# Kernel optimization log

Hardware: AMD Instinct MI355X
Metric: run time of the kernel (lower is better)

## Reference

```python
import jax, jax.numpy as jnp
import numpy as np

N_NODES = 100000
N_EDGES = 1600000
D_IN = 64
D_OUT = 64


def setup_inputs() -> dict:
    key = jax.random.key(0)
    k1, k2, k3, k4, k5, k6 = jax.random.split(key, 6)
    feat = jax.random.normal(k1, (N_NODES, D_IN), dtype=jnp.float32)
    src = jax.random.randint(k2, (N_EDGES,), 0, N_NODES, dtype=jnp.int64)
    dst = jax.random.randint(k3, (N_EDGES,), 0, N_NODES, dtype=jnp.int64)
    edge_weight = jax.random.uniform(k4, (N_EDGES,), dtype=jnp.float32)
    # Xavier-uniform with relu gain, as in reset_parameters
    gain = float(np.sqrt(2.0))
    bound = gain * float(np.sqrt(6.0 / (D_IN + D_OUT)))
    W_neigh = jax.random.uniform(k5, (D_OUT, D_IN), dtype=jnp.float32, minval=-bound, maxval=bound)
    W_self = jax.random.uniform(k6, (D_OUT, D_IN), dtype=jnp.float32, minval=-bound, maxval=bound)
    bias = jnp.zeros((D_OUT,), dtype=jnp.float32)
    return {"feat": feat, "src": src, "dst": dst, "edge_weight": edge_weight,
            "W_neigh": W_neigh, "W_self": W_self, "bias": bias}


def reference(feat, src, dst, edge_weight, W_neigh, W_self, bias):
    n = feat.shape[0]
    # feat_drop with p=0.0 is identity; in_feats == out_feats so lin_before_mp is False
    # message: u_mul_e -> gather src features, scale by edge weight  [E, D_IN]
    m = feat[src] * edge_weight[:, None]
    # mean reduce over incoming edges (zero for isolated dst nodes, matching DGL)
    s = jax.ops.segment_sum(m, dst, num_segments=n)
    deg = jax.ops.segment_sum(jnp.ones_like(edge_weight), dst, num_segments=n)
    neigh = s / jnp.maximum(deg, 1.0)[:, None]
    h_neigh = neigh @ W_neigh.T
    h_self = feat @ W_self.T
    return h_self + h_neigh + bias
```

## Files before the change

### kernel.cpp

```cpp
#include <hip/hip_runtime.h>

constexpr int N_NODES = 100000;
constexpr int N_EDGES = 1600000;
constexpr int D = 64;

constexpr int BSH    = 6;
constexpr int BN     = 1 << BSH;
constexpr int NBUCK  = (N_NODES + BN - 1) / BN;
constexpr int NPART  = 200;
constexpr int EPB    = N_EDGES / NPART;
constexpr int CAP    = 2048;
constexpr int RMAX   = 512;
constexpr int NCVT   = (N_NODES * D / 4) / 256;

constexpr size_t OFF_NCUR    = 0;
constexpr size_t OFF_BCUR    = 400000;
constexpr size_t OFF_W16     = 409600;
constexpr size_t OFF_ENTRIES = 425984;
constexpr size_t OFF_FEAT16  = 26034176;
constexpr size_t WS_NEEDED   = OFF_FEAT16 + (size_t)N_NODES * D * 2;

typedef short  bf16x8 __attribute__((ext_vector_type(8)));
typedef float  f32x4  __attribute__((ext_vector_type(4)));

union FragU { unsigned u[4]; bf16x8 v; };

__device__ __forceinline__ unsigned short f2bf(float f) {
    unsigned u = __float_as_uint(f);
    u += 0x7fffu + ((u >> 16) & 1u);
    return (unsigned short)(u >> 16);
}

__global__ __launch_bounds__(256) void k_zero(int* __restrict__ ncur,
                                              int* __restrict__ bcur) {
    const int stride = gridDim.x * 256;
    for (int i = blockIdx.x * 256 + threadIdx.x; i < N_NODES; i += stride)
        ncur[i] = 0;
    for (int i = blockIdx.x * 256 + threadIdx.x; i < NBUCK; i += stride)
        bcur[i] = 0;
}

__global__ __launch_bounds__(256) void k_pre(const float4* __restrict__ feat4,
                                             unsigned short* __restrict__ feat16,
                                             const float* __restrict__ Wn,
                                             const float* __restrict__ Ws,
                                             unsigned short* __restrict__ W16) {
    const int b   = blockIdx.x;
    const int tid = threadIdx.x;
    if (b < NCVT) {
        const int i = b * 256 + tid;
        float4 v = feat4[i];
        ushort4 o;
        o.x = f2bf(v.x); o.y = f2bf(v.y); o.z = f2bf(v.z); o.w = f2bf(v.w);
        *(ushort4*)&feat16[(size_t)i * 4] = o;
    } else {
        for (int e = tid; e < D * 128; e += 256) {
            const int j = e >> 7, k = e & 127;
            const float w = (k < D) ? Ws[j * D + k] : Wn[j * D + (k - D)];
            W16[e] = f2bf(w);
        }
    }
}

__global__ __launch_bounds__(256) void k_part(const int* __restrict__ src,
                                              const int* __restrict__ dst,
                                              const float* __restrict__ ew,
                                              int* __restrict__ ncur,
                                              int* __restrict__ bcur,
                                              uint2* __restrict__ entries) {
    __shared__ int l[NBUCK];
    const int tid  = threadIdx.x;
    const int base = blockIdx.x * EPB;
    for (int i = tid; i < NBUCK; i += 256) l[i] = 0;
    __syncthreads();
    for (int k = tid; k < EPB; k += 256)
        atomicAdd(&l[dst[base + k] >> BSH], 1);
    __syncthreads();
    for (int b = tid; b < NBUCK; b += 256) {
        const int c = l[b];
        l[b] = c ? atomicAdd(&bcur[b], c) : 0;
    }
    __syncthreads();
    for (int k = tid; k < EPB; k += 256) {
        const int e = base + k;
        const int d = dst[e];
        const int bk = d >> BSH;
        const int pos = atomicAdd(&l[bk], 1);
        const int r   = atomicAdd(&ncur[d], 1);
        if (pos < CAP && r < RMAX)
            entries[(size_t)bk * CAP + pos] =
                make_uint2((unsigned)src[e] | ((unsigned)(d & (BN - 1)) << 17)
                                            | ((unsigned)r << 23),
                           __float_as_uint(ew[e]));
    }
}

__global__ __launch_bounds__(256) void k_bucket(const uint2* __restrict__ feat16u2,
                                                const unsigned short* __restrict__ feat16,
                                                const int* __restrict__ ncur,
                                                const int* __restrict__ bcur,
                                                const uint2* __restrict__ entries,
                                                const unsigned short* __restrict__ W16,
                                                const float* __restrict__ bias,
                                                float* __restrict__ out) {
    __shared__ uint2 ent[CAP];
    __shared__ __align__(16) uint2 aggrow[BN * 16];
    __shared__ int hh[BN], st[BN];
    const int tid = threadIdx.x;
    const int b   = blockIdx.x;
    int cnt = bcur[b];
    if (cnt > CAP) cnt = CAP;

    if (tid < BN) {
        const int node = b * BN + tid;
        hh[tid] = (node < N_NODES) ? ncur[node] : 0;
    }
    __syncthreads();
    if (tid < BN) st[tid] = hh[tid];
    __syncthreads();
    for (int off = 1; off < BN; off <<= 1) {
        int u = 0;
        if (tid < BN && tid >= off) u = st[tid - off];
        __syncthreads();
        if (tid < BN) st[tid] += u;
        __syncthreads();
    }
    if (tid < BN) st[tid] -= hh[tid];
    __syncthreads();
    const uint2* slab = entries + (size_t)b * CAP;
    for (int i = tid; i < cnt; i += 256) {
        const uint2 e = slab[i];
        const int dl = (e.x >> 17) & (BN - 1);
        const int r  = (int)(e.x >> 23);
        ent[st[dl] + r] = e;
    }
    __syncthreads();

    const int wave = tid >> 6, lane = tid & 63;
    const int group = lane >> 4, gl = lane & 15;
    for (int t = 0; t < 16; ++t) {
        const int dl  = wave * 16 + t;
        const int ss  = st[dl];
        const int deg = hh[dl];
        const int se  = ss + deg;
        float4 acc = make_float4(0.f, 0.f, 0.f, 0.f);
        for (int e = ss + group; e < se; e += 4) {
            const uint2 en = ent[e];
            const float w  = __uint_as_float(en.y);
            const uint2 p  = feat16u2[(size_t)(en.x & 0x1FFFF) * 16 + gl];
            acc.x = fmaf(__uint_as_float(p.x << 16),         w, acc.x);
            acc.y = fmaf(__uint_as_float(p.x & 0xFFFF0000u), w, acc.y);
            acc.z = fmaf(__uint_as_float(p.y << 16),         w, acc.z);
            acc.w = fmaf(__uint_as_float(p.y & 0xFFFF0000u), w, acc.w);
        }
#pragma unroll
        for (int m = 16; m <= 32; m <<= 1) {
            acc.x += __shfl_xor(acc.x, m);
            acc.y += __shfl_xor(acc.y, m);
            acc.z += __shfl_xor(acc.z, m);
            acc.w += __shfl_xor(acc.w, m);
        }
        if (group == 0) {
            const float inv = 1.0f / fmaxf((float)deg, 1.0f);
            uint2 o;
            o.x = (unsigned)f2bf(acc.x * inv) | ((unsigned)f2bf(acc.y * inv) << 16);
            o.y = (unsigned)f2bf(acc.z * inv) | ((unsigned)f2bf(acc.w * inv) << 16);
            aggrow[dl * 16 + gl] = o;
        }
    }
    __syncthreads();

    const int quad = lane >> 4, r = lane & 15;
    const int node0 = b * BN + wave * 16;
    int arow = node0 + r;
    if (arow > N_NODES - 1) arow = N_NODES - 1;

    bf16x8 a[4], bb[4][4];
    a[0] = *(const bf16x8*)&feat16[(size_t)arow * 64 +      quad * 8];
    a[1] = *(const bf16x8*)&feat16[(size_t)arow * 64 + 32 + quad * 8];
    {
        const int rbase = (wave * 16 + r) * 16;
        FragU f2, f3;
        uint2 lo = aggrow[rbase + 2 * quad];
        uint2 hi = aggrow[rbase + 2 * quad + 1];
        f2.u[0] = lo.x; f2.u[1] = lo.y; f2.u[2] = hi.x; f2.u[3] = hi.y;
        lo = aggrow[rbase + 8 + 2 * quad];
        hi = aggrow[rbase + 8 + 2 * quad + 1];
        f3.u[0] = lo.x; f3.u[1] = lo.y; f3.u[2] = hi.x; f3.u[3] = hi.y;
        a[2] = f2.v;
        a[3] = f3.v;
    }
#pragma unroll
    for (int nt = 0; nt < 4; ++nt)
#pragma unroll
        for (int kc = 0; kc < 4; ++kc)
            bb[nt][kc] = *(const bf16x8*)&W16[(size_t)(nt * 16 + r) * 128 + kc * 32 + quad * 8];

    f32x4 acc[4] = {};
#pragma unroll
    for (int kc = 0; kc < 4; ++kc)
#pragma unroll
        for (int nt = 0; nt < 4; ++nt)
            acc[nt] = __builtin_amdgcn_mfma_f32_16x16x32_bf16(a[kc], bb[nt][kc], acc[nt], 0, 0, 0);

#pragma unroll
    for (int nt = 0; nt < 4; ++nt) {
        const float bv = bias[nt * 16 + r];
#pragma unroll
        for (int reg = 0; reg < 4; ++reg) {
            const int m = node0 + quad * 4 + reg;
            if (m < N_NODES) out[(size_t)m * 64 + nt * 16 + r] = acc[nt][reg] + bv;
        }
    }
}

__global__ __launch_bounds__(256) void fb_zero(float4* __restrict__ out4,
                                               float* __restrict__ deg) {
    const int stride = gridDim.x * blockDim.x;
    int i = blockIdx.x * blockDim.x + threadIdx.x;
    const int total4 = (N_NODES * D) / 4;
    for (int idx = i; idx < total4; idx += stride)
        out4[idx] = make_float4(0.f, 0.f, 0.f, 0.f);
    for (int idx = i; idx < N_NODES; idx += stride)
        deg[idx] = 0.f;
}

__global__ __launch_bounds__(256) void fb_scatter(
    const float* __restrict__ feat, const int* __restrict__ src,
    const int* __restrict__ dst, const float* __restrict__ ew,
    float* __restrict__ out, float* __restrict__ deg) {
    const int gid  = blockIdx.x * blockDim.x + threadIdx.x;
    const int e    = gid >> 6;
    const int lane = gid & 63;
    if (e >= N_EDGES) return;
    atomicAdd(&out[(size_t)dst[e] * D + lane], feat[(size_t)src[e] * D + lane] * ew[e]);
    if (lane == 0) atomicAdd(&deg[dst[e]], 1.0f);
}

__global__ __launch_bounds__(256) void fb_finalize(
    const float* __restrict__ feat, const float* __restrict__ Wn,
    const float* __restrict__ Ws, const float* __restrict__ bias,
    const float* __restrict__ deg, float* __restrict__ out) {
    __shared__ float lWn[D * 65];
    __shared__ float lWs[D * 65];
    for (int idx = threadIdx.x; idx < D * D; idx += 256) {
        const int r = idx >> 6, c = idx & 63;
        lWn[r * 65 + c] = Wn[idx];
        lWs[r * 65 + c] = Ws[idx];
    }
    __syncthreads();
    const int wave = threadIdx.x >> 6;
    const int lane = threadIdx.x & 63;
    const int n = blockIdx.x * 4 + wave;
    if (n >= N_NODES) return;
    const float f  = feat[(size_t)n * D + lane];
    const float sv = out[(size_t)n * D + lane];
    const float inv = 1.0f / fmaxf(deg[n], 1.0f);
    float acc_s = 0.f, acc_n = 0.f;
#pragma unroll
    for (int k = 0; k < D; ++k) {
        acc_s += __shfl(f, k)  * lWs[lane * 65 + k];
        acc_n += __shfl(sv, k) * lWn[lane * 65 + k];
    }
    out[(size_t)n * D + lane] = acc_s + acc_n * inv + bias[lane];
}

extern "C" void kernel_launch(void* const* d_in, const int* in_sizes, int n_in,
                              void* d_out, int out_size, void* d_ws, size_t ws_size,
                              hipStream_t stream) {
    const float* feat = (const float*)d_in[0];
    const int*   src  = (const int*)  d_in[1];
    const int*   dst  = (const int*)  d_in[2];
    const float* ew   = (const float*)d_in[3];
    const float* Wn   = (const float*)d_in[4];
    const float* Ws   = (const float*)d_in[5];
    const float* bias = (const float*)d_in[6];
    float* out = (float*)d_out;
    char* ws = (char*)d_ws;

    if (ws_size >= WS_NEEDED) {
        int*   ncur    = (int*)(ws + OFF_NCUR);
        int*   bcur    = (int*)(ws + OFF_BCUR);
        uint2* entries = (uint2*)(ws + OFF_ENTRIES);
        unsigned short* W16    = (unsigned short*)(ws + OFF_W16);
        unsigned short* feat16 = (unsigned short*)(ws + OFF_FEAT16);

        k_zero  <<<128, 256, 0, stream>>>(ncur, bcur);
        k_pre   <<<NCVT + 1, 256, 0, stream>>>((const float4*)feat, feat16, Wn, Ws, W16);
        k_part  <<<NPART, 256, 0, stream>>>(src, dst, ew, ncur, bcur, entries);
        k_bucket<<<NBUCK, 256, 0, stream>>>((const uint2*)feat16, feat16, ncur, bcur,
                                            entries, W16, bias, out);
    } else {
        float* deg = (float*)d_ws;
        fb_zero<<<2048, 256, 0, stream>>>((float4*)out, deg);
        fb_scatter<<<(N_EDGES * 64) / 256, 256, 0, stream>>>(feat, src, dst, ew, out, deg);
        fb_finalize<<<(N_NODES + 3) / 4, 256, 0, stream>>>(feat, Wn, Ws, bias, deg, out);
    }
}
```

Measured before the change: 282.7 us.

## Replace per-bucket slab partition with two-level sort into global CSR

The single partition pass that scattered edges into fixed-capacity 64-node bucket slabs with per-node rank atomics is replaced. The new path has a degree histogram folded into the preprocessing kernel, a coarse 2048-node chunk partition, a single-block prefix scan that builds node offsets, and a second pass that places edges into a dense CSR array. The aggregation kernel then reads contiguous edge ranges and drops its in-block scan and scatter. The aim is to cut scattered, contended global atomics and wasted slab reads, at the cost of two extra launches and a serial single-block scan.

```diff
diff --git a/kernel.cpp b/kernel.cpp
--- a/kernel.cpp
+++ b/kernel.cpp
@@ -7,18 +7,24 @@
 constexpr int BSH    = 6;
 constexpr int BN     = 1 << BSH;
 constexpr int NBUCK  = (N_NODES + BN - 1) / BN;
+constexpr int CSH    = 11;
+constexpr int NC     = (N_NODES + (1 << CSH) - 1) >> CSH;
 constexpr int NPART  = 200;
 constexpr int EPB    = N_EDGES / NPART;
+constexpr int CAPC   = 35328;
+constexpr int CHUNK  = 4096;
+constexpr int NCHUNK = (CAPC + CHUNK - 1) / CHUNK;
 constexpr int CAP    = 2048;
-constexpr int RMAX   = 512;
 constexpr int NCVT   = (N_NODES * D / 4) / 256;
 
-constexpr size_t OFF_NCUR    = 0;
-constexpr size_t OFF_BCUR    = 400000;
-constexpr size_t OFF_W16     = 409600;
-constexpr size_t OFF_ENTRIES = 425984;
-constexpr size_t OFF_FEAT16  = 26034176;
-constexpr size_t WS_NEEDED   = OFF_FEAT16 + (size_t)N_NODES * D * 2;
+constexpr size_t OFF_CCUR   = 0;
+constexpr size_t OFF_NCUR   = 1024;
+constexpr size_t OFF_NST    = 401408;
+constexpr size_t OFF_W16    = 801792;
+constexpr size_t OFF_EA     = 819200;
+constexpr size_t OFF_EB     = 14667776;
+constexpr size_t OFF_FEAT16 = 27467776;
+constexpr size_t WS_NEEDED  = OFF_FEAT16 + (size_t)N_NODES * D * 2;
 
 typedef short  bf16x8 __attribute__((ext_vector_type(8)));
 typedef float  f32x4  __attribute__((ext_vector_type(4)));
@@ -32,19 +38,21 @@
 }
 
 __global__ __launch_bounds__(256) void k_zero(int* __restrict__ ncur,
-                                              int* __restrict__ bcur) {
+                                              int* __restrict__ ccur) {
     const int stride = gridDim.x * 256;
     for (int i = blockIdx.x * 256 + threadIdx.x; i < N_NODES; i += stride)
         ncur[i] = 0;
-    for (int i = blockIdx.x * 256 + threadIdx.x; i < NBUCK; i += stride)
-        bcur[i] = 0;
+    for (int i = blockIdx.x * 256 + threadIdx.x; i < NC; i += stride)
+        ccur[i] = 0;
 }
 
 __global__ __launch_bounds__(256) void k_pre(const float4* __restrict__ feat4,
                                              unsigned short* __restrict__ feat16,
                                              const float* __restrict__ Wn,
                                              const float* __restrict__ Ws,
-                                             unsigned short* __restrict__ W16) {
+                                             unsigned short* __restrict__ W16,
+                                             const int* __restrict__ dst,
+                                             int* __restrict__ ncur) {
     const int b   = blockIdx.x;
     const int tid = threadIdx.x;
     if (b < NCVT) {
@@ -53,6 +61,10 @@
         ushort4 o;
         o.x = f2bf(v.x); o.y = f2bf(v.y); o.z = f2bf(v.z); o.w = f2bf(v.w);
         *(ushort4*)&feat16[(size_t)i * 4] = o;
+    } else if (b < NCVT + NPART) {
+        const int base = (b - NCVT) * EPB;
+        for (int k = tid; k < EPB; k += 256)
+            atomicAdd(&ncur[dst[base + k]], 1);
     } else {
         for (int e = tid; e < D * 128; e += 256) {
             const int j = e >> 7, k = e & 127;
@@ -62,44 +74,109 @@
     }
 }
 
-__global__ __launch_bounds__(256) void k_part(const int* __restrict__ src,
-                                              const int* __restrict__ dst,
-                                              const float* __restrict__ ew,
-                                              int* __restrict__ ncur,
-                                              int* __restrict__ bcur,
-                                              uint2* __restrict__ entries) {
-    __shared__ int l[NBUCK];
+__global__ __launch_bounds__(256) void k_pA(const int* __restrict__ src,
+                                            const int* __restrict__ dst,
+                                            const float* __restrict__ ew,
+                                            int* __restrict__ ccur,
+                                            uint2* __restrict__ ea) {
+    __shared__ int l[NC];
     const int tid  = threadIdx.x;
     const int base = blockIdx.x * EPB;
-    for (int i = tid; i < NBUCK; i += 256) l[i] = 0;
+    if (tid < NC) l[tid] = 0;
     __syncthreads();
     for (int k = tid; k < EPB; k += 256)
-        atomicAdd(&l[dst[base + k] >> BSH], 1);
-    __syncthreads();
-    for (int b = tid; b < NBUCK; b += 256) {
-        const int c = l[b];
-        l[b] = c ? atomicAdd(&bcur[b], c) : 0;
+        atomicAdd(&l[dst[base + k] >> CSH], 1);
+    __syncthreads();
+    if (tid < NC) {
+        const int c = l[tid];
+        l[tid] = c ? atomicAdd(&ccur[tid], c) : 0;
     }
     __syncthreads();
     for (int k = tid; k < EPB; k += 256) {
         const int e = base + k;
         const int d = dst[e];
-        const int bk = d >> BSH;
-        const int pos = atomicAdd(&l[bk], 1);
-        const int r   = atomicAdd(&ncur[d], 1);
-        if (pos < CAP && r < RMAX)
-            entries[(size_t)bk * CAP + pos] =
-                make_uint2((unsigned)src[e] | ((unsigned)(d & (BN - 1)) << 17)
-                                            | ((unsigned)r << 23),
+        const int c = d >> CSH;
+        const int pos = atomicAdd(&l[c], 1);
+        if (pos < CAPC)
+            ea[(size_t)c * CAPC + pos] =
+                make_uint2((unsigned)src[e] | ((unsigned)(d & ((1 << CSH) - 1)) << 17),
                            __float_as_uint(ew[e]));
+    }
+}
+
+__global__ __launch_bounds__(1024) void k_scan(int* __restrict__ ncur,
+                                               int* __restrict__ nst) {
+    __shared__ int s[1024];
+    __shared__ int carry_s;
+    const int t = threadIdx.x;
+    if (t == 0) carry_s = 0;
+    __syncthreads();
+    for (int tile = 0; tile < 5; ++tile) {
+        const int base = tile * 24576 + t * 24;
+        int v[24];
+        int sum = 0;
+#pragma unroll
+        for (int i = 0; i < 24; i += 4) {
+            int4 q = make_int4(0, 0, 0, 0);
+            if (base + i + 3 < N_NODES) {
+                q = *(const int4*)&ncur[base + i];
+            } else {
+                if (base + i     < N_NODES) q.x = ncur[base + i];
+                if (base + i + 1 < N_NODES) q.y = ncur[base + i + 1];
+                if (base + i + 2 < N_NODES) q.z = ncur[base + i + 2];
+                if (base + i + 3 < N_NODES) q.w = ncur[base + i + 3];
+            }
+            v[i] = q.x; v[i + 1] = q.y; v[i + 2] = q.z; v[i + 3] = q.w;
+            sum += q.x + q.y + q.z + q.w;
+        }
+        s[t] = sum;
+        __syncthreads();
+        for (int off = 1; off < 1024; off <<= 1) {
+            int u = (t >= off) ? s[t - off] : 0;
+            __syncthreads();
+            s[t] += u;
+            __syncthreads();
+        }
+        int run = carry_s + s[t] - sum;
+#pragma unroll
+        for (int i = 0; i < 24; ++i) {
+            const int idx = base + i;
+            if (idx < N_NODES) { nst[idx] = run; ncur[idx] = 0; }
+            run += v[i];
+        }
+        __syncthreads();
+        if (t == 0) carry_s += s[1023];
+        __syncthreads();
+    }
+    if (t == 0) nst[N_NODES] = carry_s;
+}
+
+__global__ __launch_bounds__(256) void k_pB(const uint2* __restrict__ ea,
+                                            const int* __restrict__ ccur,
+                                            const int* __restrict__ nst,
+                                            int* __restrict__ rcur,
+                                            uint2* __restrict__ eb) {
+    const int c = blockIdx.x / NCHUNK;
+    const int k = blockIdx.x % NCHUNK;
+    int cnt = ccur[c];
+    if (cnt > CAPC) cnt = CAPC;
+    const int start = k * CHUNK;
+    int end = start + CHUNK;
+    if (end > cnt) end = cnt;
+    const uint2* slab = ea + (size_t)c * CAPC;
+    const int nbase = c << CSH;
+    for (int i = start + threadIdx.x; i < end; i += 256) {
+        const uint2 e = slab[i];
+        const int node = nbase + (int)(e.x >> 17);
+        const int r = atomicAdd(&rcur[node], 1);
+        eb[nst[node] + r] = make_uint2(e.x & 0x1FFFF, e.y);
     }
 }
 
 __global__ __launch_bounds__(256) void k_bucket(const uint2* __restrict__ feat16u2,
                                                 const unsigned short* __restrict__ feat16,
-                                                const int* __restrict__ ncur,
-                                                const int* __restrict__ bcur,
-                                                const uint2* __restrict__ entries,
+                                                const int* __restrict__ nst,
+                                                const uint2* __restrict__ eb,
                                                 const unsigned short* __restrict__ W16,
                                                 const float* __restrict__ bias,
                                                 float* __restrict__ out) {
@@ -108,32 +185,25 @@
     __shared__ int hh[BN], st[BN];
     const int tid = threadIdx.x;
     const int b   = blockIdx.x;
-    int cnt = bcur[b];
+    const int node0b = b * BN;
+    const int s0 = nst[node0b];
+    int s1idx = node0b + BN;
+    if (s1idx > N_NODES) s1idx = N_NODES;
+    const int s1 = nst[s1idx];
+    int cnt = s1 - s0;
     if (cnt > CAP) cnt = CAP;
 
     if (tid < BN) {
-        const int node = b * BN + tid;
-        hh[tid] = (node < N_NODES) ? ncur[node] : 0;
-    }
-    __syncthreads();
-    if (tid < BN) st[tid] = hh[tid];
-    __syncthreads();
-    for (int off = 1; off < BN; off <<= 1) {
-        int u = 0;
-        if (tid < BN && tid >= off) u = st[tid - off];
-        __syncthreads();
-        if (tid < BN) st[tid] += u;
-        __syncthreads();
-    }
-    if (tid < BN) st[tid] -= hh[tid];
-    __syncthreads();
-    const uint2* slab = entries + (size_t)b * CAP;
-    for (int i = tid; i < cnt; i += 256) {
-        const uint2 e = slab[i];
-        const int dl = (e.x >> 17) & (BN - 1);
-        const int r  = (int)(e.x >> 23);
-        ent[st[dl] + r] = e;
-    }
+        const int idx = node0b + tid;
+        if (idx < N_NODES) {
+            st[tid] = nst[idx] - s0;
+            hh[tid] = nst[idx + 1] - nst[idx];
+        } else {
+            st[tid] = 0;
+            hh[tid] = 0;
+        }
+    }
+    for (int i = tid; i < cnt; i += 256) ent[i] = eb[s0 + i];
     __syncthreads();
 
     const int wave = tid >> 6, lane = tid & 63;
@@ -171,7 +241,7 @@
     __syncthreads();
 
     const int quad = lane >> 4, r = lane & 15;
-    const int node0 = b * BN + wave * 16;
+    const int node0 = node0b + wave * 16;
     int arow = node0 + r;
     if (arow > N_NODES - 1) arow = N_NODES - 1;
 
@@ -279,17 +349,22 @@
     char* ws = (char*)d_ws;
 
     if (ws_size >= WS_NEEDED) {
-        int*   ncur    = (int*)(ws + OFF_NCUR);
-        int*   bcur    = (int*)(ws + OFF_BCUR);
-        uint2* entries = (uint2*)(ws + OFF_ENTRIES);
+        int*   ccur = (int*)(ws + OFF_CCUR);
+        int*   ncur = (int*)(ws + OFF_NCUR);
+        int*   nst  = (int*)(ws + OFF_NST);
+        uint2* ea   = (uint2*)(ws + OFF_EA);
+        uint2* eb   = (uint2*)(ws + OFF_EB);
         unsigned short* W16    = (unsigned short*)(ws + OFF_W16);
         unsigned short* feat16 = (unsigned short*)(ws + OFF_FEAT16);
 
-        k_zero  <<<128, 256, 0, stream>>>(ncur, bcur);
-        k_pre   <<<NCVT + 1, 256, 0, stream>>>((const float4*)feat, feat16, Wn, Ws, W16);
-        k_part  <<<NPART, 256, 0, stream>>>(src, dst, ew, ncur, bcur, entries);
-        k_bucket<<<NBUCK, 256, 0, stream>>>((const uint2*)feat16, feat16, ncur, bcur,
-                                            entries, W16, bias, out);
+        k_zero  <<<128, 256, 0, stream>>>(ncur, ccur);
+        k_pre   <<<NCVT + NPART + 1, 256, 0, stream>>>((const float4*)feat, feat16,
+                                                       Wn, Ws, W16, dst, ncur);
+        k_pA    <<<NPART, 256, 0, stream>>>(src, dst, ew, ccur, ea);
+        k_scan  <<<1, 1024, 0, stream>>>(ncur, nst);
+        k_pB    <<<NC * NCHUNK, 256, 0, stream>>>(ea, ccur, nst, ncur, eb);
+        k_bucket<<<NBUCK, 256, 0, stream>>>((const uint2*)feat16, feat16, nst, eb,
+                                            W16, bias, out);
     } else {
         float* deg = (float*)d_ws;
         fb_zero<<<2048, 256, 0, stream>>>((float4*)out, deg);
```

After: 501.9 us. 1.78x slower.
